# Kernel tuning notes

Measured on AMD Instinct MI355X. Metric: run time of the kernel, lower is better.

The kernel has to match this reference:

```python
import jax, jax.numpy as jnp
import numpy as np

B, NB, NA, D, PF = 16384, 8, 16, 128, 1
IN_DIM = D + NA * D + D  # basis + flattened sf + task = 2304
QK_DIM = D * 3 * PF      # 384
V_DIM = D * PF           # 128


def rbf_similarity(x, y):
    # RBF kernel over the feature axis: exp(-0.5 * ||x - y||^2)
    return jnp.exp(-0.5 * jnp.sum((x - y) ** 2, axis=-1))


def setup_inputs() -> dict:
    key = jax.random.key(0)
    ks = jax.random.split(key, 9)
    basis = jax.random.normal(ks[0], (B, NB, D), dtype=jnp.float32)
    sf_all = jax.random.normal(ks[1], (B, NB, NA, D), dtype=jnp.float32)
    task = jax.random.normal(ks[2], (B, NB, D), dtype=jnp.float32)
    mask = (jax.random.uniform(ks[3], (B, NB, D * PF)) > 0.5).astype(jnp.float32)
    s_in = 1.0 / np.sqrt(IN_DIM)
    s_v = 1.0 / np.sqrt(D)
    Wq = jax.random.normal(ks[4], (IN_DIM, QK_DIM), dtype=jnp.float32) * s_in
    Wk = jax.random.normal(ks[5], (IN_DIM, QK_DIM), dtype=jnp.float32) * s_in
    bk = jnp.zeros((QK_DIM,), dtype=jnp.float32)
    Wv = jax.random.normal(ks[6], (D, V_DIM), dtype=jnp.float32) * s_v
    bv = jnp.zeros((V_DIM,), dtype=jnp.float32)
    return {"basis_features_all": basis, "sf_all": sf_all, "task": task, "mask": mask,
            "Wq": Wq, "Wk": Wk, "bk": bk, "Wv": Wv, "bv": bv}


def reference(basis_features_all, sf_all, task, mask, Wq, Wk, bk, Wv, bv):
    b = sf_all.shape[0]
    sf_all_r = jnp.reshape(sf_all, (b, NB, NA * D))          # (B, NB, NA*D)
    sf_first_r = sf_all_r[:, :1, :]                          # (B, 1, NA*D)
    task = jax.lax.stop_gradient(task)
    task_n = task / jnp.linalg.norm(task, ord=2, axis=-1, keepdims=True)

    # RBF similarity side-branch between consecutive beakers
    bst = jnp.concatenate([basis_features_all, sf_all_r, task_n], axis=-1)  # (B, NB, IN_DIM)
    sim = rbf_similarity(bst[:, :-1, :], bst[:, 1:, :]).mean(axis=0)        # (NB-1,)

    bf_first = basis_features_all[:, :1, :]
    bf_rest = jax.lax.stop_gradient(basis_features_all[:, 1:, :])
    bf_all = jnp.concatenate([bf_first, bf_rest], axis=1)

    q_in = jnp.concatenate([bf_first, sf_first_r, task_n[:, :1, :]], axis=-1)  # (B, 1, IN_DIM)
    query = q_in @ Wq                                                          # (B, 1, QK)
    k_in = jnp.concatenate([bf_all, sf_all_r, task_n], axis=-1)                # (B, NB, IN_DIM)
    keys = k_in @ Wk + bk                                                      # (B, NB, QK)
    values = sf_all @ Wv + bv                                                  # (B, NB, NA, V)

    mask_rep = jnp.repeat(mask, 3, axis=-1)                                    # (B, NB, QK)
    keys_masked = keys * mask_rep
    values_masked = values

    attn_logits = jnp.matmul(query, jnp.swapaxes(keys_masked, -2, -1)) / jnp.sqrt(jnp.float32(D * PF))
    attn_logits = jnp.where(attn_logits == 0, -1e9, attn_logits)               # zero-mask trick
    attention_weights = jax.nn.softmax(attn_logits, axis=-1)                   # (B, 1, NB)

    attended_sf = jnp.einsum('bna,baqf->bnqf', attention_weights, values_masked)  # (B, 1, NA, V)
    task_first = task[:, 0, :]                                                    # (B, D)
    q_1 = jnp.einsum('bi,bnji->bj', task_first, attended_sf)                      # (B, NA)
    return (q_1, attended_sf, attn_logits, attention_weights, keys_masked, values_masked, sim)
```

## Files before the change

### kernel.cpp

```cpp
#include <hip/hip_runtime.h>
#include <hip/hip_bf16.h>
#include <math.h>

static constexpr size_t OFF_ATT = 262144;
static constexpr size_t OFF_LOG = 33816576;
static constexpr size_t OFF_W   = 33947648;
static constexpr size_t OFF_KM  = 34078720;
static constexpr size_t OFF_VM  = 84410368;
static constexpr size_t OFF_SIM = 352845824;

typedef short bf16x8 __attribute__((ext_vector_type(8)));
typedef float f32x4 __attribute__((ext_vector_type(4)));

__device__ inline unsigned short f2bf(float f) {
  union { float f; unsigned u; } x; x.f = f;
  unsigned r = x.u + 0x7FFFu + ((x.u >> 16) & 1u);
  return (unsigned short)(r >> 16);
}

__device__ inline float wave_sum(float v) {
#pragma unroll
  for (int o = 32; o > 0; o >>= 1) v += __shfl_xor(v, o, 64);
  return v;
}

__global__ void norm_kernel(const float* __restrict__ task, float* __restrict__ invn,
                            float* __restrict__ simo) {
  int idx = blockIdx.x * 4 + (threadIdx.x >> 6);
  int lane = threadIdx.x & 63;
  float t0 = task[(size_t)idx * 128 + lane];
  float t1 = task[(size_t)idx * 128 + 64 + lane];
  float s = wave_sum(t0 * t0 + t1 * t1);
  if (lane == 0) invn[idx] = rsqrtf(s);
  if (blockIdx.x == 0 && threadIdx.x < 7) simo[threadIdx.x] = 0.0f;
}

__global__ void wprep_t(const float* __restrict__ W, unsigned short* __restrict__ WT,
                        int K, int N) {
  int ntn = N >> 6;
  int kt = blockIdx.x / ntn, nt = blockIdx.x % ntn;
  int k0 = kt * 64, n0 = nt * 64;
  __shared__ float t[64][65];
  int tid = threadIdx.x;
  int r = tid >> 2, c0 = (tid & 3) * 16;
#pragma unroll
  for (int q = 0; q < 4; ++q) {
    float4 v = *(const float4*)(W + (size_t)(k0 + r) * N + n0 + c0 + q * 4);
    t[r][c0 + q * 4 + 0] = v.x; t[r][c0 + q * 4 + 1] = v.y;
    t[r][c0 + q * 4 + 2] = v.z; t[r][c0 + q * 4 + 3] = v.w;
  }
  __syncthreads();
  int n = tid >> 2, kc0 = (tid & 3) * 16;
#pragma unroll
  for (int q = 0; q < 4; ++q) {
    int kc = kc0 + q * 4;
    ushort4 o = make_ushort4(f2bf(t[kc + 0][n]), f2bf(t[kc + 1][n]),
                             f2bf(t[kc + 2][n]), f2bf(t[kc + 3][n]));
    *(ushort4*)(WT + (size_t)(n0 + n) * K + k0 + kc) = o;
  }
}

__global__ __launch_bounds__(576) void abuild_sim(const float* __restrict__ basis,
                                                  const float* __restrict__ sf,
                                                  const float* __restrict__ task,
                                                  const float* __restrict__ invn,
                                                  unsigned short* __restrict__ Abf,
                                                  float* __restrict__ simo) {
  int b = blockIdx.x;
  int f = threadIdx.x;
  size_t row0 = (size_t)b * 8;
  float4 v[8];
#pragma unroll
  for (int n = 0; n < 8; ++n) {
    size_t row = row0 + n;
    float4 x;
    if (f < 32)       x = *(const float4*)(basis + row * 128 + f * 4);
    else if (f < 544) x = *(const float4*)(sf + row * 2048 + (f - 32) * 4);
    else {
      x = *(const float4*)(task + row * 128 + (f - 544) * 4);
      float s = invn[row];
      x.x *= s; x.y *= s; x.z *= s; x.w *= s;
    }
    v[n] = x;
    ushort4 o = make_ushort4(f2bf(x.x), f2bf(x.y), f2bf(x.z), f2bf(x.w));
    *(ushort4*)(Abf + row * 2304 + f * 4) = o;
  }
  float s7[7];
#pragma unroll
  for (int n = 1; n < 8; ++n) {
    float dx = v[n].x - v[n - 1].x, dy = v[n].y - v[n - 1].y;
    float dz = v[n].z - v[n - 1].z, dw = v[n].w - v[n - 1].w;
    s7[n - 1] = dx * dx + dy * dy + dz * dz + dw * dw;
  }
  __shared__ float red[9][7];
  int wid = threadIdx.x >> 6, lane = threadIdx.x & 63;
#pragma unroll
  for (int i = 0; i < 7; ++i) {
    float p = wave_sum(s7[i]);
    if (lane == 0) red[wid][i] = p;
  }
  __syncthreads();
  if (threadIdx.x < 7) {
    float s = 0.f;
#pragma unroll
    for (int w = 0; w < 9; ++w) s += red[w][threadIdx.x];
    atomicAdd(&simo[threadIdx.x], expf(-0.5f * s) * (1.0f / 16384.0f));
  }
}

template <int MODE>
__global__ __launch_bounds__(256) void qk_gemm(const unsigned short* __restrict__ Abf,
                                               const unsigned short* __restrict__ WT,
                                               const float* __restrict__ bias,
                                               const float* __restrict__ mask,
                                               float* __restrict__ outp) {
  __shared__ unsigned short As[128 * 40];
  __shared__ unsigned short Bs[128 * 40];
  int nwg = gridDim.x, per = nwg >> 3;
  int bid = blockIdx.x;
  int swz = (bid & 7) * per + (bid >> 3);
  int mt = swz / 3, nt = swz - mt * 3;
  int tid = threadIdx.x;
  int wave = tid >> 6, lane = tid & 63;
  int wr = wave >> 1, wc = wave & 1;
  int r = tid >> 1, h = tid & 1;

  f32x4 acc[4][4];
#pragma unroll
  for (int i = 0; i < 4; ++i)
#pragma unroll
    for (int j = 0; j < 4; ++j) acc[i][j] = (f32x4)(0.f);

  size_t arow = (MODE == 1) ? (size_t)(mt * 128 + r) * 8 : (size_t)(mt * 128 + r);
  const unsigned short* aptr = Abf + arow * 2304 + h * 16;
  const unsigned short* bptr = WT + (size_t)(nt * 128 + r) * 2304 + h * 16;
  int la = lane & 15, lk = (lane >> 4) * 8;

  bf16x8 a0 = *(const bf16x8*)(aptr);
  bf16x8 a1 = *(const bf16x8*)(aptr + 8);
  bf16x8 b0 = *(const bf16x8*)(bptr);
  bf16x8 b1 = *(const bf16x8*)(bptr + 8);

  for (int ks = 0; ks < 72; ++ks) {
    *(bf16x8*)(As + r * 40 + h * 16)     = a0;
    *(bf16x8*)(As + r * 40 + h * 16 + 8) = a1;
    *(bf16x8*)(Bs + r * 40 + h * 16)     = b0;
    *(bf16x8*)(Bs + r * 40 + h * 16 + 8) = b1;
    __syncthreads();
    if (ks < 71) {
      int k1 = (ks + 1) * 32;
      a0 = *(const bf16x8*)(aptr + k1);
      a1 = *(const bf16x8*)(aptr + k1 + 8);
      b0 = *(const bf16x8*)(bptr + k1);
      b1 = *(const bf16x8*)(bptr + k1 + 8);
    }
    bf16x8 af[4], bf[4];
#pragma unroll
    for (int mi = 0; mi < 4; ++mi)
      af[mi] = *(const bf16x8*)(As + (wr * 64 + mi * 16 + la) * 40 + lk);
#pragma unroll
    for (int ni = 0; ni < 4; ++ni)
      bf[ni] = *(const bf16x8*)(Bs + (wc * 64 + ni * 16 + la) * 40 + lk);
#pragma unroll
    for (int mi = 0; mi < 4; ++mi)
#pragma unroll
      for (int ni = 0; ni < 4; ++ni)
        acc[mi][ni] = __builtin_amdgcn_mfma_f32_16x16x32_bf16(af[mi], bf[ni], acc[mi][ni], 0, 0, 0);
    __syncthreads();
  }

  int rq = lane >> 4;
#pragma unroll
  for (int mi = 0; mi < 4; ++mi) {
#pragma unroll
    for (int ni = 0; ni < 4; ++ni) {
      int colg = nt * 128 + wc * 64 + ni * 16 + la;
#pragma unroll
      for (int j = 0; j < 4; ++j) {
        int rowg = mt * 128 + wr * 64 + mi * 16 + rq * 4 + j;
        float v = acc[mi][ni][j];
        if (MODE == 0)
          v = (v + bias[colg]) * mask[(size_t)rowg * 128 + (unsigned)colg / 3u];
        outp[(size_t)rowg * 384 + colg] = v;
      }
    }
  }
}

__global__ void attn_kernel(const float* __restrict__ query, const float* __restrict__ km,
                            float* __restrict__ logits, float* __restrict__ wts) {
  int b = blockIdx.x;
  int tid = threadIdx.x;
  int w = tid >> 6, lane = tid & 63;
  __shared__ float lg[8];
  __shared__ float post[8];
  __shared__ float ex[8];
  for (int n = w; n < 8; n += 4) {
    float p = 0.f;
    for (int k = lane; k < 384; k += 64)
      p += query[(size_t)b * 384 + k] * km[((size_t)b * 8 + n) * 384 + k];
    p = wave_sum(p);
    if (lane == 0) lg[n] = p * 0.08838834764831845f;
  }
  __syncthreads();
  if (tid < 8) {
    float l = lg[tid];
    l = (l == 0.0f) ? -1e9f : l;
    post[tid] = l;
    logits[(size_t)b * 8 + tid] = l;
  }
  __syncthreads();
  if (tid < 8) {
    float m = post[0];
#pragma unroll
    for (int i = 1; i < 8; ++i) m = fmaxf(m, post[i]);
    ex[tid] = expf(post[tid] - m);
  }
  __syncthreads();
  if (tid < 8) {
    float s = 0.f;
#pragma unroll
    for (int i = 0; i < 8; ++i) s += ex[i];
    wts[(size_t)b * 8 + tid] = ex[tid] / s;
  }
}

__global__ __launch_bounds__(256) void v_gemm_attend(const float* __restrict__ sf,
                                                     const float* __restrict__ Wv,
                                                     const float* __restrict__ bv,
                                                     const float* __restrict__ wts,
                                                     const float* __restrict__ task,
                                                     float* __restrict__ vm,
                                                     float* __restrict__ att,
                                                     float* __restrict__ q1) {
  __shared__ unsigned short As[128 * 40];
  __shared__ unsigned short Bs[128 * 136];
  float* attL = (float*)As;
  int bid = blockIdx.x;
  int swz = (bid & 7) * 2048 + (bid >> 3);
  int b = swz;
  size_t m0 = (size_t)swz * 128;
  int tid = threadIdx.x;
  int wave = tid >> 6, lane = tid & 63;
  int wr = wave >> 1, wc = wave & 1;
  int r = tid >> 1, h = tid & 1;
  int la = lane & 15, lkq = lane >> 4;

#pragma unroll
  for (int q = 0; q < 16; ++q) {
    int flat = q * 256 + tid;
    int k = flat >> 5;
    int n4 = (flat & 31) * 4;
    float4 v = *(const float4*)(Wv + (size_t)k * 128 + n4);
    Bs[(n4 + 0) * 136 + k] = f2bf(v.x);
    Bs[(n4 + 1) * 136 + k] = f2bf(v.y);
    Bs[(n4 + 2) * 136 + k] = f2bf(v.z);
    Bs[(n4 + 3) * 136 + k] = f2bf(v.w);
  }

  f32x4 acc[4][4];
#pragma unroll
  for (int i = 0; i < 4; ++i)
#pragma unroll
    for (int j = 0; j < 4; ++j) acc[i][j] = (f32x4)(0.f);

  for (int ks = 0; ks < 4; ++ks) {
    int k0 = ks * 32;
    const float* ap = sf + (m0 + r) * 128 + k0 + h * 16;
    float4 v0 = *(const float4*)(ap);
    float4 v1 = *(const float4*)(ap + 4);
    float4 v2 = *(const float4*)(ap + 8);
    float4 v3 = *(const float4*)(ap + 12);
    ushort4 p0 = make_ushort4(f2bf(v0.x), f2bf(v0.y), f2bf(v0.z), f2bf(v0.w));
    ushort4 p1 = make_ushort4(f2bf(v1.x), f2bf(v1.y), f2bf(v1.z), f2bf(v1.w));
    ushort4 p2 = make_ushort4(f2bf(v2.x), f2bf(v2.y), f2bf(v2.z), f2bf(v2.w));
    ushort4 p3 = make_ushort4(f2bf(v3.x), f2bf(v3.y), f2bf(v3.z), f2bf(v3.w));
    *(ushort4*)(As + r * 40 + h * 16)      = p0;
    *(ushort4*)(As + r * 40 + h * 16 + 4)  = p1;
    *(ushort4*)(As + r * 40 + h * 16 + 8)  = p2;
    *(ushort4*)(As + r * 40 + h * 16 + 12) = p3;
    __syncthreads();
    bf16x8 af[4], bfr[4];
#pragma unroll
    for (int mi = 0; mi < 4; ++mi)
      af[mi] = *(const bf16x8*)(As + (wr * 64 + mi * 16 + la) * 40 + lkq * 8);
#pragma unroll
    for (int ni = 0; ni < 4; ++ni)
      bfr[ni] = *(const bf16x8*)(Bs + (wc * 64 + ni * 16 + la) * 136 + k0 + lkq * 8);
#pragma unroll
    for (int mi = 0; mi < 4; ++mi)
#pragma unroll
      for (int ni = 0; ni < 4; ++ni)
        acc[mi][ni] = __builtin_amdgcn_mfma_f32_16x16x32_bf16(af[mi], bfr[ni], acc[mi][ni], 0, 0, 0);
    __syncthreads();
  }

  float w4[4];
#pragma unroll
  for (int mi = 0; mi < 4; ++mi) w4[mi] = wts[(size_t)b * 8 + wr * 4 + mi];
  float pacc[4][4];
#pragma unroll
  for (int ni = 0; ni < 4; ++ni)
#pragma unroll
    for (int j = 0; j < 4; ++j) pacc[ni][j] = 0.f;
#pragma unroll
  for (int mi = 0; mi < 4; ++mi) {
#pragma unroll
    for (int ni = 0; ni < 4; ++ni) {
      int colg = wc * 64 + ni * 16 + la;
      float bb = bv[colg];
#pragma unroll
      for (int j = 0; j < 4; ++j) {
        size_t rowg = m0 + wr * 64 + mi * 16 + lkq * 4 + j;
        float v = acc[mi][ni][j] + bb;
        vm[rowg * 128 + colg] = v;
        pacc[ni][j] = fmaf(w4[mi], v, pacc[ni][j]);
      }
    }
  }
  if (wr == 0) {
#pragma unroll
    for (int ni = 0; ni < 4; ++ni)
#pragma unroll
      for (int j = 0; j < 4; ++j)
        attL[(lkq * 4 + j) * 132 + wc * 64 + ni * 16 + la] = pacc[ni][j];
  }
  __syncthreads();
  if (wr == 1) {
#pragma unroll
    for (int ni = 0; ni < 4; ++ni)
#pragma unroll
      for (int j = 0; j < 4; ++j)
        attL[(lkq * 4 + j) * 132 + wc * 64 + ni * 16 + la] += pacc[ni][j];
  }
  __syncthreads();
#pragma unroll
  for (int i = 0; i < 2; ++i) {
    int fidx = tid + i * 256;
    int a = fidx >> 5, c = (fidx & 31) * 4;
    f32x4 vv = *(const f32x4*)(attL + a * 132 + c);
    *(f32x4*)(att + (size_t)b * 2048 + a * 128 + c) = vv;
  }
  for (int j = wave; j < 16; j += 4) {
    float p = task[(size_t)b * 1024 + lane] * attL[j * 132 + lane]
            + task[(size_t)b * 1024 + 64 + lane] * attL[j * 132 + 64 + lane];
    p = wave_sum(p);
    if (lane == 0) q1[(size_t)b * 16 + j] = p;
  }
}

extern "C" void kernel_launch(void* const* d_in, const int* in_sizes, int n_in,
                              void* d_out, int out_size, void* d_ws, size_t ws_size,
                              hipStream_t stream) {
  const float* basis = (const float*)d_in[0];
  const float* sf    = (const float*)d_in[1];
  const float* task  = (const float*)d_in[2];
  const float* mask  = (const float*)d_in[3];
  const float* Wq    = (const float*)d_in[4];
  const float* Wk    = (const float*)d_in[5];
  const float* bk    = (const float*)d_in[6];
  const float* Wv    = (const float*)d_in[7];
  const float* bv    = (const float*)d_in[8];

  float* out  = (float*)d_out;
  float* q1   = out;
  float* att  = out + OFF_ATT;
  float* logi = out + OFF_LOG;
  float* wts  = out + OFF_W;
  float* km   = out + OFF_KM;
  float* vm   = out + OFF_VM;
  float* simo = out + OFF_SIM;

  float* query = att;
  float* invn  = att + 6291456;
  unsigned short* WkT = (unsigned short*)(att + 6422528);
  unsigned short* WqT = WkT + 884736;
  unsigned short* Abf = (unsigned short*)vm;

  norm_kernel<<<32768, 256, 0, stream>>>(task, invn, simo);
  wprep_t<<<216, 256, 0, stream>>>(Wk, WkT, 2304, 384);
  wprep_t<<<216, 256, 0, stream>>>(Wq, WqT, 2304, 384);
  abuild_sim<<<16384, 576, 0, stream>>>(basis, sf, task, invn, Abf, simo);
  qk_gemm<0><<<3072, 256, 0, stream>>>(Abf, WkT, bk, mask, km);
  qk_gemm<1><<<384, 256, 0, stream>>>(Abf, WqT, nullptr, nullptr, query);
  attn_kernel<<<16384, 256, 0, stream>>>(query, km, logi, wts);
  v_gemm_attend<<<16384, 256, 0, stream>>>(sf, Wv, bv, wts, task, vm, att, q1);
}
```

Measured before the change: 1.448 ms.

## Use direct global-to-LDS loads with double-buffered shared tiles in QK GEMM

The QK GEMM now fills LDS with global_load_lds (direct global-to-shared DMA) instead of staging through registers, and double-buffers the A/B tiles so the next K-slice loads while MFMAs run on the current one. This drops the register round trip and one barrier per iteration. The LDS layout loses its 40-element padded row stride and becomes a dense 32-element stride, which can cause bank conflicts on fragment reads. Correctness relies on the synchronisation point ordering the async LDS writes, and shared memory use doubles.

```diff
diff --git a/kernel.cpp b/kernel.cpp
--- a/kernel.cpp
+++ b/kernel.cpp
@@ -114,8 +114,8 @@
                                                const float* __restrict__ bias,
                                                const float* __restrict__ mask,
                                                float* __restrict__ outp) {
-  __shared__ unsigned short As[128 * 40];
-  __shared__ unsigned short Bs[128 * 40];
+  __shared__ unsigned short As[2 * 4096];
+  __shared__ unsigned short Bs[2 * 4096];
   int nwg = gridDim.x, per = nwg >> 3;
   int bid = blockIdx.x;
   int swz = (bid & 7) * per + (bid >> 3);
@@ -123,7 +123,39 @@
   int tid = threadIdx.x;
   int wave = tid >> 6, lane = tid & 63;
   int wr = wave >> 1, wc = wave & 1;
-  int r = tid >> 1, h = tid & 1;
+  int m0g = mt * 128, n0g = nt * 128;
+
+  int c_lo = wave * 2 * 64 + lane;
+  int row_q0 = c_lo >> 2, kc_q0 = (c_lo & 3) * 8;
+  int c_hi = c_lo + 64;
+  int row_q1 = c_hi >> 2, kc_q1 = (c_hi & 3) * 8;
+  size_t ga_q0 = (MODE == 1) ? (size_t)(m0g + row_q0) * 8 : (size_t)(m0g + row_q0);
+  size_t ga_q1 = (MODE == 1) ? (size_t)(m0g + row_q1) * 8 : (size_t)(m0g + row_q1);
+  const unsigned short* ag0 = Abf + ga_q0 * 2304 + kc_q0;
+  const unsigned short* ag1 = Abf + ga_q1 * 2304 + kc_q1;
+  const unsigned short* bg0 = WT + (size_t)(n0g + row_q0) * 2304 + kc_q0;
+  const unsigned short* bg1 = WT + (size_t)(n0g + row_q1) * 2304 + kc_q1;
+  int ldsoff0 = wave * 2 * 512;
+  int ldsoff1 = ldsoff0 + 512;
+
+#define STAGE(ks, cur)                                                                   \
+  do {                                                                                   \
+    int _k0 = (ks) * 32;                                                                 \
+    unsigned short* _a = As + (cur) * 4096;                                              \
+    unsigned short* _b = Bs + (cur) * 4096;                                              \
+    __builtin_amdgcn_global_load_lds(                                                    \
+        (const __attribute__((address_space(1))) void*)(ag0 + _k0),                      \
+        (__attribute__((address_space(3))) void*)(_a + ldsoff0), 16, 0, 0);              \
+    __builtin_amdgcn_global_load_lds(                                                    \
+        (const __attribute__((address_space(1))) void*)(ag1 + _k0),                      \
+        (__attribute__((address_space(3))) void*)(_a + ldsoff1), 16, 0, 0);              \
+    __builtin_amdgcn_global_load_lds(                                                    \
+        (const __attribute__((address_space(1))) void*)(bg0 + _k0),                      \
+        (__attribute__((address_space(3))) void*)(_b + ldsoff0), 16, 0, 0);              \
+    __builtin_amdgcn_global_load_lds(                                                    \
+        (const __attribute__((address_space(1))) void*)(bg1 + _k0),                      \
+        (__attribute__((address_space(3))) void*)(_b + ldsoff1), 16, 0, 0);              \
+  } while (0)
 
   f32x4 acc[4][4];
 #pragma unroll
@@ -131,43 +163,31 @@
 #pragma unroll
     for (int j = 0; j < 4; ++j) acc[i][j] = (f32x4)(0.f);
 
-  size_t arow = (MODE == 1) ? (size_t)(mt * 128 + r) * 8 : (size_t)(mt * 128 + r);
-  const unsigned short* aptr = Abf + arow * 2304 + h * 16;
-  const unsigned short* bptr = WT + (size_t)(nt * 128 + r) * 2304 + h * 16;
   int la = lane & 15, lk = (lane >> 4) * 8;
 
-  bf16x8 a0 = *(const bf16x8*)(aptr);
-  bf16x8 a1 = *(const bf16x8*)(aptr + 8);
-  bf16x8 b0 = *(const bf16x8*)(bptr);
-  bf16x8 b1 = *(const bf16x8*)(bptr + 8);
-
+  STAGE(0, 0);
+  __syncthreads();
+  int cur = 0;
   for (int ks = 0; ks < 72; ++ks) {
-    *(bf16x8*)(As + r * 40 + h * 16)     = a0;
-    *(bf16x8*)(As + r * 40 + h * 16 + 8) = a1;
-    *(bf16x8*)(Bs + r * 40 + h * 16)     = b0;
-    *(bf16x8*)(Bs + r * 40 + h * 16 + 8) = b1;
-    __syncthreads();
-    if (ks < 71) {
-      int k1 = (ks + 1) * 32;
-      a0 = *(const bf16x8*)(aptr + k1);
-      a1 = *(const bf16x8*)(aptr + k1 + 8);
-      b0 = *(const bf16x8*)(bptr + k1);
-      b1 = *(const bf16x8*)(bptr + k1 + 8);
-    }
+    if (ks < 71) STAGE(ks + 1, cur ^ 1);
+    const unsigned short* aL = As + cur * 4096;
+    const unsigned short* bL = Bs + cur * 4096;
     bf16x8 af[4], bf[4];
 #pragma unroll
     for (int mi = 0; mi < 4; ++mi)
-      af[mi] = *(const bf16x8*)(As + (wr * 64 + mi * 16 + la) * 40 + lk);
+      af[mi] = *(const bf16x8*)(aL + (wr * 64 + mi * 16 + la) * 32 + lk);
 #pragma unroll
     for (int ni = 0; ni < 4; ++ni)
-      bf[ni] = *(const bf16x8*)(Bs + (wc * 64 + ni * 16 + la) * 40 + lk);
+      bf[ni] = *(const bf16x8*)(bL + (wc * 64 + ni * 16 + la) * 32 + lk);
 #pragma unroll
     for (int mi = 0; mi < 4; ++mi)
 #pragma unroll
       for (int ni = 0; ni < 4; ++ni)
         acc[mi][ni] = __builtin_amdgcn_mfma_f32_16x16x32_bf16(af[mi], bf[ni], acc[mi][ni], 0, 0, 0);
     __syncthreads();
-  }
+    cur ^= 1;
+  }
+#undef STAGE
 
   int rq = lane >> 4;
 #pragma unroll
```

Result: faster. 1.401 ms (-3.2%).

## Fuse A-matrix build and RBF similarity into the QK GEMM with double buffering

Applied to the files above, without the earlier changes.

Removes the separate abuild_sim kernel. Before, it converted basis/sf/normalized-task rows to a bf16 A matrix in global memory, which the GEMM then read back. Now the GEMM loads fp32 inputs directly, scales the task segment by the inverse norm, converts to bf16 into LDS, and accumulates the consecutive-row squared distances for the similarity in the nt==0 blocks. B tiles are staged straight into LDS with global_load_lds, and A/B LDS buffers are double-buffered, so each k-step needs one barrier instead of two. This avoids writing and re-reading the intermediate bf16 matrix, but each of the three N-tiles now re-reads fp32 A data (twice the bytes of bf16) and register pressure rises.

```diff
diff --git a/kernel.cpp b/kernel.cpp
--- a/kernel.cpp
+++ b/kernel.cpp
@@ -60,62 +60,15 @@
   }
 }
 
-__global__ __launch_bounds__(576) void abuild_sim(const float* __restrict__ basis,
-                                                  const float* __restrict__ sf,
-                                                  const float* __restrict__ task,
-                                                  const float* __restrict__ invn,
-                                                  unsigned short* __restrict__ Abf,
-                                                  float* __restrict__ simo) {
-  int b = blockIdx.x;
-  int f = threadIdx.x;
-  size_t row0 = (size_t)b * 8;
-  float4 v[8];
-#pragma unroll
-  for (int n = 0; n < 8; ++n) {
-    size_t row = row0 + n;
-    float4 x;
-    if (f < 32)       x = *(const float4*)(basis + row * 128 + f * 4);
-    else if (f < 544) x = *(const float4*)(sf + row * 2048 + (f - 32) * 4);
-    else {
-      x = *(const float4*)(task + row * 128 + (f - 544) * 4);
-      float s = invn[row];
-      x.x *= s; x.y *= s; x.z *= s; x.w *= s;
-    }
-    v[n] = x;
-    ushort4 o = make_ushort4(f2bf(x.x), f2bf(x.y), f2bf(x.z), f2bf(x.w));
-    *(ushort4*)(Abf + row * 2304 + f * 4) = o;
-  }
-  float s7[7];
-#pragma unroll
-  for (int n = 1; n < 8; ++n) {
-    float dx = v[n].x - v[n - 1].x, dy = v[n].y - v[n - 1].y;
-    float dz = v[n].z - v[n - 1].z, dw = v[n].w - v[n - 1].w;
-    s7[n - 1] = dx * dx + dy * dy + dz * dz + dw * dw;
-  }
-  __shared__ float red[9][7];
-  int wid = threadIdx.x >> 6, lane = threadIdx.x & 63;
-#pragma unroll
-  for (int i = 0; i < 7; ++i) {
-    float p = wave_sum(s7[i]);
-    if (lane == 0) red[wid][i] = p;
-  }
-  __syncthreads();
-  if (threadIdx.x < 7) {
-    float s = 0.f;
-#pragma unroll
-    for (int w = 0; w < 9; ++w) s += red[w][threadIdx.x];
-    atomicAdd(&simo[threadIdx.x], expf(-0.5f * s) * (1.0f / 16384.0f));
-  }
-}
-
 template <int MODE>
-__global__ __launch_bounds__(256) void qk_gemm(const unsigned short* __restrict__ Abf,
-                                               const unsigned short* __restrict__ WT,
-                                               const float* __restrict__ bias,
-                                               const float* __restrict__ mask,
-                                               float* __restrict__ outp) {
-  __shared__ unsigned short As[128 * 40];
-  __shared__ unsigned short Bs[128 * 40];
+__global__ __launch_bounds__(256) void qk_gemm_fused(
+    const float* __restrict__ basis, const float* __restrict__ sf,
+    const float* __restrict__ task, const float* __restrict__ invn,
+    const unsigned short* __restrict__ WT, const float* __restrict__ bias,
+    const float* __restrict__ mask, float* __restrict__ outp,
+    float* __restrict__ simo) {
+  __shared__ unsigned short As[2 * 5120];
+  __shared__ unsigned short Bs[2 * 4096];
   int nwg = gridDim.x, per = nwg >> 3;
   int bid = blockIdx.x;
   int swz = (bid & 7) * per + (bid >> 3);
@@ -123,7 +76,111 @@
   int tid = threadIdx.x;
   int wave = tid >> 6, lane = tid & 63;
   int wr = wave >> 1, wc = wave & 1;
-  int r = tid >> 1, h = tid & 1;
+  int m0g = mt * 128, n0g = nt * 128;
+  int la = lane & 15, lk = (lane >> 4) * 8;
+
+  int c_lo = wave * 128 + lane;
+  int brow0 = c_lo >> 2, bkc0 = (c_lo & 3) * 8;
+  int c_hi = c_lo + 64;
+  int brow1 = c_hi >> 2, bkc1 = (c_hi & 3) * 8;
+  const unsigned short* bg0 = WT + (size_t)(n0g + brow0) * 2304 + bkc0;
+  const unsigned short* bg1 = WT + (size_t)(n0g + brow1) * 2304 + bkc1;
+  int ldsB0 = wave * 1024;
+  int ldsB1 = ldsB0 + 512;
+
+  int p = tid & 63, part = tid >> 6;
+  int r0 = 2 * p, r1 = r0 + 1;
+  constexpr bool SIM = (MODE == 0);
+  bool do_sim = SIM && (nt == 0);
+  bool has_odd = do_sim && ((p & 3) != 3);
+  size_t R0 = (MODE == 1) ? (size_t)(m0g + r0) * 8 : (size_t)(m0g + r0);
+  size_t R1 = (MODE == 1) ? (size_t)(m0g + r1) * 8 : (size_t)(m0g + r1);
+  size_t R2 = has_odd ? (size_t)(m0g + r0 + 2) : R1;
+  float iv0 = invn[R0], iv1 = invn[R1], iv2 = invn[R2];
+  int kofs = part * 8;
+
+  float4 a00 = {0,0,0,0}, a01 = {0,0,0,0}, a10 = {0,0,0,0}, a11 = {0,0,0,0};
+  float4 a20 = {0,0,0,0}, a21 = {0,0,0,0};
+  float sa = 0.f, sb = 0.f;
+
+  auto LOADA = [&](int k0) {
+    const float *q0, *q1, *q2;
+    bool sc = false;
+    if (k0 < 128) {
+      q0 = basis + R0 * 128 + k0 + kofs;
+      q1 = basis + R1 * 128 + k0 + kofs;
+      q2 = basis + R2 * 128 + k0 + kofs;
+    } else if (k0 < 2176) {
+      int kk = k0 - 128 + kofs;
+      q0 = sf + R0 * 2048 + kk;
+      q1 = sf + R1 * 2048 + kk;
+      q2 = sf + R2 * 2048 + kk;
+    } else {
+      int kk = k0 - 2176 + kofs;
+      q0 = task + R0 * 128 + kk;
+      q1 = task + R1 * 128 + kk;
+      q2 = task + R2 * 128 + kk;
+      sc = true;
+    }
+    a00 = *(const float4*)q0; a01 = *(const float4*)(q0 + 4);
+    a10 = *(const float4*)q1; a11 = *(const float4*)(q1 + 4);
+    if (has_odd) { a20 = *(const float4*)q2; a21 = *(const float4*)(q2 + 4); }
+    if (sc) {
+      a00.x *= iv0; a00.y *= iv0; a00.z *= iv0; a00.w *= iv0;
+      a01.x *= iv0; a01.y *= iv0; a01.z *= iv0; a01.w *= iv0;
+      a10.x *= iv1; a10.y *= iv1; a10.z *= iv1; a10.w *= iv1;
+      a11.x *= iv1; a11.y *= iv1; a11.z *= iv1; a11.w *= iv1;
+      if (has_odd) {
+        a20.x *= iv2; a20.y *= iv2; a20.z *= iv2; a20.w *= iv2;
+        a21.x *= iv2; a21.y *= iv2; a21.z *= iv2; a21.w *= iv2;
+      }
+    }
+  };
+
+  auto SIMACC = [&]() {
+    if (!do_sim) return;
+    float d;
+    d = a00.x - a10.x; sa = fmaf(d, d, sa);
+    d = a00.y - a10.y; sa = fmaf(d, d, sa);
+    d = a00.z - a10.z; sa = fmaf(d, d, sa);
+    d = a00.w - a10.w; sa = fmaf(d, d, sa);
+    d = a01.x - a11.x; sa = fmaf(d, d, sa);
+    d = a01.y - a11.y; sa = fmaf(d, d, sa);
+    d = a01.z - a11.z; sa = fmaf(d, d, sa);
+    d = a01.w - a11.w; sa = fmaf(d, d, sa);
+    if (has_odd) {
+      d = a10.x - a20.x; sb = fmaf(d, d, sb);
+      d = a10.y - a20.y; sb = fmaf(d, d, sb);
+      d = a10.z - a20.z; sb = fmaf(d, d, sb);
+      d = a10.w - a20.w; sb = fmaf(d, d, sb);
+      d = a11.x - a21.x; sb = fmaf(d, d, sb);
+      d = a11.y - a21.y; sb = fmaf(d, d, sb);
+      d = a11.z - a21.z; sb = fmaf(d, d, sb);
+      d = a11.w - a21.w; sb = fmaf(d, d, sb);
+    }
+  };
+
+  auto CVTW = [&](int cb) {
+    unsigned short* aL = As + cb * 5120;
+    bf16x8 u = { (short)f2bf(a00.x), (short)f2bf(a00.y), (short)f2bf(a00.z), (short)f2bf(a00.w),
+                 (short)f2bf(a01.x), (short)f2bf(a01.y), (short)f2bf(a01.z), (short)f2bf(a01.w) };
+    bf16x8 v = { (short)f2bf(a10.x), (short)f2bf(a10.y), (short)f2bf(a10.z), (short)f2bf(a10.w),
+                 (short)f2bf(a11.x), (short)f2bf(a11.y), (short)f2bf(a11.z), (short)f2bf(a11.w) };
+    *(bf16x8*)(aL + r0 * 40 + kofs) = u;
+    *(bf16x8*)(aL + r1 * 40 + kofs) = v;
+  };
+
+#define STAGE_B(ks, cb)                                                        \
+  do {                                                                         \
+    __builtin_amdgcn_global_load_lds(                                          \
+        (const __attribute__((address_space(1))) void*)(bg0 + (ks) * 32),      \
+        (__attribute__((address_space(3))) void*)(Bs + (cb) * 4096 + ldsB0),   \
+        16, 0, 0);                                                             \
+    __builtin_amdgcn_global_load_lds(                                          \
+        (const __attribute__((address_space(1))) void*)(bg1 + (ks) * 32),      \
+        (__attribute__((address_space(3))) void*)(Bs + (cb) * 4096 + ldsB1),   \
+        16, 0, 0);                                                             \
+  } while (0)
 
   f32x4 acc[4][4];
 #pragma unroll
@@ -131,43 +188,42 @@
 #pragma unroll
     for (int j = 0; j < 4; ++j) acc[i][j] = (f32x4)(0.f);
 
-  size_t arow = (MODE == 1) ? (size_t)(mt * 128 + r) * 8 : (size_t)(mt * 128 + r);
-  const unsigned short* aptr = Abf + arow * 2304 + h * 16;
-  const unsigned short* bptr = WT + (size_t)(nt * 128 + r) * 2304 + h * 16;
-  int la = lane & 15, lk = (lane >> 4) * 8;
-
-  bf16x8 a0 = *(const bf16x8*)(aptr);
-  bf16x8 a1 = *(const bf16x8*)(aptr + 8);
-  bf16x8 b0 = *(const bf16x8*)(bptr);
-  bf16x8 b1 = *(const bf16x8*)(bptr + 8);
-
+  LOADA(0);
+  STAGE_B(0, 0);
+  SIMACC();
+  CVTW(0);
+  __syncthreads();
+
+  int cur = 0;
   for (int ks = 0; ks < 72; ++ks) {
-    *(bf16x8*)(As + r * 40 + h * 16)     = a0;
-    *(bf16x8*)(As + r * 40 + h * 16 + 8) = a1;
-    *(bf16x8*)(Bs + r * 40 + h * 16)     = b0;
-    *(bf16x8*)(Bs + r * 40 + h * 16 + 8) = b1;
+    if (ks < 71) {
+      LOADA((ks + 1) * 32);
+      STAGE_B(ks + 1, cur ^ 1);
+    }
+    {
+      const unsigned short* aL = As + cur * 5120;
+      const unsigned short* bL = Bs + cur * 4096;
+      bf16x8 af[4], bfr[4];
+#pragma unroll
+      for (int mi = 0; mi < 4; ++mi)
+        af[mi] = *(const bf16x8*)(aL + (wr * 64 + mi * 16 + la) * 40 + lk);
+#pragma unroll
+      for (int ni = 0; ni < 4; ++ni)
+        bfr[ni] = *(const bf16x8*)(bL + (wc * 64 + ni * 16 + la) * 32 + lk);
+#pragma unroll
+      for (int mi = 0; mi < 4; ++mi)
+#pragma unroll
+        for (int ni = 0; ni < 4; ++ni)
+          acc[mi][ni] = __builtin_amdgcn_mfma_f32_16x16x32_bf16(af[mi], bfr[ni], acc[mi][ni], 0, 0, 0);
+    }
+    if (ks < 71) {
+      SIMACC();
+      CVTW(cur ^ 1);
+    }
     __syncthreads();
-    if (ks < 71) {
-      int k1 = (ks + 1) * 32;
-      a0 = *(const bf16x8*)(aptr + k1);
-      a1 = *(const bf16x8*)(aptr + k1 + 8);
-      b0 = *(const bf16x8*)(bptr + k1);
-      b1 = *(const bf16x8*)(bptr + k1 + 8);
-    }
-    bf16x8 af[4], bf[4];
-#pragma unroll
-    for (int mi = 0; mi < 4; ++mi)
-      af[mi] = *(const bf16x8*)(As + (wr * 64 + mi * 16 + la) * 40 + lk);
-#pragma unroll
-    for (int ni = 0; ni < 4; ++ni)
-      bf[ni] = *(const bf16x8*)(Bs + (wc * 64 + ni * 16 + la) * 40 + lk);
-#pragma unroll
-    for (int mi = 0; mi < 4; ++mi)
-#pragma unroll
-      for (int ni = 0; ni < 4; ++ni)
-        acc[mi][ni] = __builtin_amdgcn_mfma_f32_16x16x32_bf16(af[mi], bf[ni], acc[mi][ni], 0, 0, 0);
-    __syncthreads();
-  }
+    cur ^= 1;
+  }
+#undef STAGE_B
 
   int rq = lane >> 4;
 #pragma unroll
@@ -182,6 +238,24 @@
         if (MODE == 0)
           v = (v + bias[colg]) * mask[(size_t)rowg * 128 + (unsigned)colg / 3u];
         outp[(size_t)rowg * 384 + colg] = v;
+      }
+    }
+  }
+
+  if (SIM) {
+    if (do_sim) {
+      float* sred = (float*)Bs;
+      sred[part * 64 + p] = sa;
+      sred[256 + part * 64 + p] = sb;
+      __syncthreads();
+      if (tid < 128) {
+        int odd = tid >> 6, pp = tid & 63;
+        if (!(odd && ((pp & 3) == 3))) {
+          float s = sred[odd * 256 + pp] + sred[odd * 256 + 64 + pp] +
+                    sred[odd * 256 + 128 + pp] + sred[odd * 256 + 192 + pp];
+          int n = (2 * pp + odd) & 7;
+          atomicAdd(&simo[n], expf(-0.5f * s) * (1.0f / 16384.0f));
+        }
       }
     }
   }
@@ -375,14 +449,12 @@
   float* invn  = att + 6291456;
   unsigned short* WkT = (unsigned short*)(att + 6422528);
   unsigned short* WqT = WkT + 884736;
-  unsigned short* Abf = (unsigned short*)vm;
 
   norm_kernel<<<32768, 256, 0, stream>>>(task, invn, simo);
   wprep_t<<<216, 256, 0, stream>>>(Wk, WkT, 2304, 384);
   wprep_t<<<216, 256, 0, stream>>>(Wq, WqT, 2304, 384);
-  abuild_sim<<<16384, 576, 0, stream>>>(basis, sf, task, invn, Abf, simo);
-  qk_gemm<0><<<3072, 256, 0, stream>>>(Abf, WkT, bk, mask, km);
-  qk_gemm<1><<<384, 256, 0, stream>>>(Abf, WqT, nullptr, nullptr, query);
+  qk_gemm_fused<0><<<3072, 256, 0, stream>>>(basis, sf, task, invn, WkT, bk, mask, km, simo);
+  qk_gemm_fused<1><<<384, 256, 0, stream>>>(basis, sf, task, invn, WqT, nullptr, nullptr, query, nullptr);
   attn_kernel<<<16384, 256, 0, stream>>>(query, km, logi, wts);
   v_gemm_attend<<<16384, 256, 0, stream>>>(sf, Wv, bv, wts, task, vm, att, q1);
 }
```

Result: slower. 1.538 ms (+6.2%).
